# Kernel optimization log

Hardware: AMD Instinct MI355X
Metric: run time of the kernel (lower is better)

Reference implementation:

```python
import jax, jax.numpy as jnp
import numpy as np

B, T, C, H = 2, 2048, 2048, 16
HD = C // H


def setup_inputs() -> dict:
    key = jax.random.key(0)
    ks = jax.random.split(key, 5)
    s = 0.02  # init scale for weights
    return {
        "x": jax.random.normal(ks[0], (B, T, C), jnp.float32),
        "Wq": jax.random.normal(ks[1], (C, C), jnp.float32) * s,
        "Wk": jax.random.normal(ks[2], (C, C), jnp.float32) * s,
        "Wv": jax.random.normal(ks[3], (C, C), jnp.float32) * s,
        "Wo": jax.random.normal(ks[4], (C, C), jnp.float32) * s,
        "bo": jnp.zeros((C,), jnp.float32),
    }


def _alibi_slopes(n_head):
    # power-of-2 path of _get_alibi_slopes (n_head=16 is a power of 2)
    return jnp.array([1.0 / 2 ** (i + 1) for i in range(n_head)], jnp.float32)


def reference(x, Wq, Wk, Wv, Wo, bo):
    b, t, c = x.shape
    h, hd = H, HD
    scale = 1.0 / np.sqrt(hd)
    # nn.Linear (no bias): y = x @ W.T; split heads -> (B,H,T,HD)
    q = (x @ Wq.T).reshape(b, t, h, hd).transpose(0, 2, 1, 3)
    k = (x @ Wk.T).reshape(b, t, h, hd).transpose(0, 2, 1, 3)
    v = (x @ Wv.T).reshape(b, t, h, hd).transpose(0, 2, 1, 3)
    scores = jnp.einsum("bhtd,bhsd->bhts", q, k) * scale  # (B,H,T,T)
    pos = jnp.arange(t)
    diff = pos[:, None] - pos[None, :]  # (T,T), i-j
    slopes = _alibi_slopes(h)
    bias = slopes[:, None, None] * diff.astype(jnp.float32)  # (H,T,T)
    causal = diff >= 0  # lower-triangular mask
    bias = jnp.where(causal[None, :, :], bias, -jnp.inf)
    scores = scores + bias[None]  # (B,H,T,T)
    attn = jax.nn.softmax(scores, axis=-1)  # dropout = identity (eval mode)
    out = jnp.einsum("bhts,bhsd->bhtd", attn, v)
    out = out.transpose(0, 2, 1, 3).reshape(b, t, c)
    out = out @ Wo.T + bo  # proj_dropout = identity (eval mode)
    return out, attn
```

## Files before the change

kernel.cpp:

```cpp
#include <hip/hip_runtime.h>
#include <hip/hip_bf16.h>

#define DEVINL __device__ __forceinline__

typedef __attribute__((ext_vector_type(8))) short bf16x8;
typedef __attribute__((ext_vector_type(4))) float f32x4;

DEVINL ushort f2bf(float f) {
  unsigned u = __float_as_uint(f);
  u += 0x7fffu + ((u >> 16) & 1u);
  return (ushort)(u >> 16);
}

DEVINL void gl_lds16(const void* g, void* lds) {
  __builtin_amdgcn_global_load_lds(
      (const __attribute__((address_space(1))) void*)g,
      (__attribute__((address_space(3))) void*)lds, 16, 0, 0);
}

DEVINL f32x4 mfma16(bf16x8 a, bf16x8 b, f32x4 c) {
  return __builtin_amdgcn_mfma_f32_16x16x32_bf16(a, b, c, 0, 0, 0);
}

__global__ __launch_bounds__(256) void cast_bf16_kernel(const float4* __restrict__ in,
                                                        ushort4* __restrict__ out, int n4) {
  int stride = (int)(gridDim.x * blockDim.x);
  for (int i = (int)(blockIdx.x * blockDim.x + threadIdx.x); i < n4; i += stride) {
    float4 v = in[i];
    out[i] = make_ushort4(f2bf(v.x), f2bf(v.y), f2bf(v.z), f2bf(v.w));
  }
}

template <int MODE>
__global__ __launch_bounds__(256) void gemm_nt(const ushort* __restrict__ A,
                                               const ushort* __restrict__ Bm,
                                               ushort* __restrict__ Qo,
                                               ushort* __restrict__ Ko,
                                               ushort* __restrict__ Vo,
                                               float* __restrict__ Fo,
                                               const float* __restrict__ bias,
                                               int M, int N, int K) {
  __shared__ __align__(16) ushort Al[2][8192];
  __shared__ __align__(16) ushort Bl[2][8192];
  const int tid = (int)threadIdx.x;
  const int l = tid & 63, w = tid >> 6;
  const int wr = w >> 1, wc = w & 1;
  const int lr = l & 15, lg = l >> 4;

  const int nwg = (int)(gridDim.x * gridDim.y);
  const int flat = (int)(blockIdx.y * gridDim.x + blockIdx.x);
  const int swz = (flat & 7) * (nwg >> 3) + (flat >> 3);
  const int bx = swz % (int)gridDim.x, by = swz / (int)gridDim.x;
  const int rowT = by * 128, colT = bx * 128;

  f32x4 acc[4][4] = {};

  auto stage = [&](int kt, int buf) {
#pragma unroll
    for (int q = 0; q < 4; ++q) {
      int s = q * 256 + tid;
      int rb = s >> 7, ks = (s >> 6) & 1, sl = s & 63;
      size_t koff = (size_t)(kt + ks * 32 + (sl >> 4) * 8);
      gl_lds16(A + (size_t)(rowT + rb * 16 + (sl & 15)) * K + koff,
               &Al[buf][(size_t)(q * 256 + (tid & 192)) * 8]);
      gl_lds16(Bm + (size_t)(colT + rb * 16 + (sl & 15)) * K + koff,
               &Bl[buf][(size_t)(q * 256 + (tid & 192)) * 8]);
    }
  };

  stage(0, 0);
  __syncthreads();
  int cur = 0;
  for (int kt = 0; kt < K; kt += 64) {
    if (kt + 64 < K) stage(kt + 64, cur ^ 1);
#pragma unroll
    for (int ks = 0; ks < 2; ++ks) {
      bf16x8 af[4], bfv[4];
#pragma unroll
      for (int i = 0; i < 4; ++i) {
        af[i]  = *(const bf16x8*)(&Al[cur][(((wr * 4 + i) * 2 + ks) * 64 + l) * 8]);
        bfv[i] = *(const bf16x8*)(&Bl[cur][(((wc * 4 + i) * 2 + ks) * 64 + l) * 8]);
      }
#pragma unroll
      for (int i = 0; i < 4; ++i)
#pragma unroll
        for (int j = 0; j < 4; ++j)
          acc[i][j] = mfma16(af[i], bfv[j], acc[i][j]);
    }
    __syncthreads();
    cur ^= 1;
  }

  const int seg = colT >> 11;
#pragma unroll
  for (int i = 0; i < 4; ++i) {
#pragma unroll
    for (int j = 0; j < 4; ++j) {
      const int col = colT + wc * 64 + j * 16 + lr;
#pragma unroll
      for (int e = 0; e < 4; ++e) {
        const int row = rowT + wr * 64 + i * 16 + lg * 4 + e;
        float v = acc[i][j][e];
        if (MODE == 3) {
          const int c = col & 2047;
          if (seg == 0)      Qo[(size_t)row * 2048 + c] = f2bf(v);
          else if (seg == 1) Ko[(size_t)row * 2048 + c] = f2bf(v);
          else               Vo[((size_t)((row >> 11) * 2048 + c)) * 2048 + (row & 2047)] = f2bf(v);
        } else {
          Fo[(size_t)row * 2048 + col] = v + bias[col];
        }
      }
    }
  }
}

__global__ __launch_bounds__(256) void flash_kernel(const ushort* __restrict__ Qg,
                                                    const ushort* __restrict__ Kg,
                                                    const ushort* __restrict__ Vt,
                                                    ushort* __restrict__ Og,
                                                    float2* __restrict__ stats) {
  __shared__ __align__(16) ushort Kl[2][8192];
  __shared__ __align__(16) ushort Vl[2][8192];
  __shared__ __align__(16) ushort Pl[4][1024];

  const int flat = (int)(blockIdx.y * gridDim.x + blockIdx.x);
  const int swz = (flat & 7) * 64 + (flat >> 3);
  const int bx = swz & 15, bh = swz >> 4;
  const int b = bh >> 4, h = bh & 15;
  const int tid = (int)threadIdx.x, l = tid & 63, w = tid >> 6;
  const int lr = l & 15, lg = l >> 4;
  const float scale = 0.08838834764831845f;
  const float slope = exp2f(-(float)(h + 1));
  const ushort* Kbase = Kg + ((size_t)b * 2048) * 2048 + h * 128;
  const ushort* Vbase = Vt + ((size_t)b * 2048 + h * 128) * 2048;

  for (int half = 0; half < 2; ++half) {
    const int qb = (half == 0) ? 31 - bx : bx;
    const int qr0 = qb * 64 + w * 16;

    bf16x8 qf[4];
#pragma unroll
    for (int ks = 0; ks < 4; ++ks)
      qf[ks] = *(const bf16x8*)(Qg + ((size_t)b * 2048 + qr0 + lr) * 2048 + h * 128 + ks * 32 + lg * 8);

    float runmax[4], runsum[4];
    f32x4 o[8] = {};
#pragma unroll
    for (int j = 0; j < 4; ++j) { runmax[j] = -__builtin_inff(); runsum[j] = 0.f; }

    auto stage = [&](int jt, int buf) {
#pragma unroll
      for (int q = 0; q < 4; ++q) {
        const int s = q * 256 + tid;
        const int sl = s & 63;
        const int cb = s >> 8, ks = (s >> 6) & 3;
        gl_lds16(Kbase + (size_t)(jt * 64 + cb * 16 + (sl & 15)) * 2048 + ks * 32 + (sl >> 4) * 8,
                 &Kl[buf][(size_t)(q * 256 + (tid & 192)) * 8]);
        const int db = s >> 7, k2 = (s >> 6) & 1;
        gl_lds16(Vbase + (size_t)(db * 16 + (sl & 15)) * 2048 + jt * 64 + k2 * 32 + (sl >> 4) * 8,
                 &Vl[buf][(size_t)(q * 256 + (tid & 192)) * 8]);
      }
    };

    stage(qb, 0);
    __syncthreads();

    for (int jt = qb; jt >= 0; --jt) {
      const int cur = (qb - jt) & 1;
      if (jt > 0) stage(jt - 1, cur ^ 1);

      f32x4 sc[4];
      __builtin_amdgcn_s_setprio(1);
#pragma unroll
      for (int cb = 0; cb < 4; ++cb) {
        f32x4 a = {};
#pragma unroll
        for (int ks = 0; ks < 4; ++ks) {
          bf16x8 kf = *(const bf16x8*)(&Kl[cur][((cb * 4 + ks) * 64 + l) * 8]);
          a = mfma16(qf[ks], kf, a);
        }
        sc[cb] = a;
      }
      __builtin_amdgcn_s_setprio(0);
#pragma unroll
      for (int cb = 0; cb < 4; ++cb) {
        const int kj = jt * 64 + cb * 16 + lr;
#pragma unroll
        for (int j = 0; j < 4; ++j) {
          const int qi = qr0 + lg * 4 + j;
          sc[cb][j] = (kj <= qi) ? sc[cb][j] * scale + slope * (float)(qi - kj) : -__builtin_inff();
        }
      }

      float nm[4];
      bool need = false;
#pragma unroll
      for (int j = 0; j < 4; ++j) {
        float m = fmaxf(fmaxf(sc[0][j], sc[1][j]), fmaxf(sc[2][j], sc[3][j]));
#pragma unroll
        for (int d = 1; d < 16; d <<= 1) m = fmaxf(m, __shfl_xor(m, d));
        nm[j] = fmaxf(runmax[j], m);
        need = need || (nm[j] > runmax[j]);
      }
      if (__any(need)) {
#pragma unroll
        for (int j = 0; j < 4; ++j) {
          const float f = __expf(runmax[j] - nm[j]);
          runsum[j] *= f;
#pragma unroll
          for (int db = 0; db < 8; ++db) o[db][j] *= f;
          runmax[j] = nm[j];
        }
      }

#pragma unroll
      for (int cb = 0; cb < 4; ++cb) {
        const int kc = cb * 16 + lr;
#pragma unroll
        for (int j = 0; j < 4; ++j) {
          const float p = __expf(sc[cb][j] - runmax[j]);
          runsum[j] += p;
          const int l2 = (((kc & 31) >> 3) << 4) | (lg * 4 + j);
          Pl[w][((kc >> 5) * 64 + l2) * 8 + (kc & 7)] = f2bf(p);
        }
      }

      bf16x8 pf0 = *(const bf16x8*)(&Pl[w][(size_t)l * 8]);
      bf16x8 pf1 = *(const bf16x8*)(&Pl[w][(size_t)(64 + l) * 8]);
      __builtin_amdgcn_s_setprio(1);
#pragma unroll
      for (int db = 0; db < 8; ++db) {
        o[db] = mfma16(pf0, *(const bf16x8*)(&Vl[cur][((db * 2 + 0) * 64 + l) * 8]), o[db]);
        o[db] = mfma16(pf1, *(const bf16x8*)(&Vl[cur][((db * 2 + 1) * 64 + l) * 8]), o[db]);
      }
      __builtin_amdgcn_s_setprio(0);
      __syncthreads();
    }

#pragma unroll
    for (int j = 0; j < 4; ++j) {
      float s = runsum[j];
#pragma unroll
      for (int d = 1; d < 16; d <<= 1) s += __shfl_xor(s, d);
      const float iv = 1.0f / s;
      if (lr == 0) stats[(size_t)bh * 2048 + qr0 + lg * 4 + j] = make_float2(runmax[j], iv);
#pragma unroll
      for (int db = 0; db < 8; ++db) o[db][j] *= iv;
    }
#pragma unroll
    for (int db = 0; db < 8; ++db)
#pragma unroll
      for (int j = 0; j < 4; ++j)
        Og[((size_t)b * 2048 + qr0 + lg * 4 + j) * 2048 + h * 128 + db * 16 + lr] = f2bf(o[db][j]);
  }
}

__global__ __launch_bounds__(256) void probs_kernel(const ushort* __restrict__ Qg,
                                                    const ushort* __restrict__ Kg,
                                                    const float2* __restrict__ stats,
                                                    float* __restrict__ attn_out) {
  const int kb = (int)blockIdx.x, qb = (int)blockIdx.y, bh = (int)blockIdx.z;
  const int tid = (int)threadIdx.x;

  if (kb > qb) {
    float* base = attn_out + ((size_t)bh * 2048 + qb * 128) * 2048 + kb * 128;
    const float4 z = make_float4(0.f, 0.f, 0.f, 0.f);
#pragma unroll
    for (int it = 0; it < 16; ++it) {
      const int idx = it * 256 + tid;
      *(float4*)(base + (size_t)(idx >> 5) * 2048 + (idx & 31) * 4) = z;
    }
    return;
  }

  __shared__ __align__(16) ushort Ql[16384];
  __shared__ __align__(16) ushort Kl[16384];
  const int b = bh >> 4, h = bh & 15;
  const int l = tid & 63, w = tid >> 6;
  const int wr = w >> 1, wc = w & 1;
  const int lr = l & 15, lg = l >> 4;
  const float scale = 0.08838834764831845f;
  const float slope = exp2f(-(float)(h + 1));

#pragma unroll
  for (int q = 0; q < 8; ++q) {
    const int s = q * 256 + tid;
    const int sl = s & 63, rb = s >> 8, ks = (s >> 6) & 3;
    const size_t koff = (size_t)(h * 128 + ks * 32 + (sl >> 4) * 8);
    gl_lds16(Qg + ((size_t)b * 2048 + qb * 128 + rb * 16 + (sl & 15)) * 2048 + koff,
             Ql + (size_t)(q * 256 + (tid & 192)) * 8);
    gl_lds16(Kg + ((size_t)b * 2048 + kb * 128 + rb * 16 + (sl & 15)) * 2048 + koff,
             Kl + (size_t)(q * 256 + (tid & 192)) * 8);
  }
  __syncthreads();

  f32x4 acc[4][4] = {};
#pragma unroll
  for (int ks = 0; ks < 4; ++ks) {
    bf16x8 af[4], bfv[4];
#pragma unroll
    for (int i = 0; i < 4; ++i) {
      af[i]  = *(const bf16x8*)(Ql + (((wr * 4 + i) * 4 + ks) * 64 + l) * 8);
      bfv[i] = *(const bf16x8*)(Kl + (((wc * 4 + i) * 4 + ks) * 64 + l) * 8);
    }
#pragma unroll
    for (int i = 0; i < 4; ++i)
#pragma unroll
      for (int j = 0; j < 4; ++j)
        acc[i][j] = mfma16(af[i], bfv[j], acc[i][j]);
  }

  float2 st[4][4];
#pragma unroll
  for (int i = 0; i < 4; ++i)
#pragma unroll
    for (int e = 0; e < 4; ++e)
      st[i][e] = stats[(size_t)bh * 2048 + qb * 128 + wr * 64 + i * 16 + lg * 4 + e];

#pragma unroll
  for (int i = 0; i < 4; ++i) {
#pragma unroll
    for (int j = 0; j < 4; ++j) {
      const int kj = kb * 128 + wc * 64 + j * 16 + lr;
#pragma unroll
      for (int e = 0; e < 4; ++e) {
        const int qi = qb * 128 + wr * 64 + i * 16 + lg * 4 + e;
        const float sv = acc[i][j][e] * scale + slope * (float)(qi - kj);
        float p = __expf(sv - st[i][e].x) * st[i][e].y;
        if (kj > qi) p = 0.f;
        attn_out[((size_t)bh * 2048 + qi) * 2048 + kj] = p;
      }
    }
  }
}

extern "C" void kernel_launch(void* const* d_in, const int* in_sizes, int n_in,
                              void* d_out, int out_size, void* d_ws, size_t ws_size,
                              hipStream_t stream) {
  (void)in_sizes; (void)n_in; (void)out_size; (void)ws_size;
  const float* x  = (const float*)d_in[0];
  const float* Wq = (const float*)d_in[1];
  const float* Wk = (const float*)d_in[2];
  const float* Wv = (const float*)d_in[3];
  const float* Wo = (const float*)d_in[4];
  const float* bo = (const float*)d_in[5];

  float* outp  = (float*)d_out;
  float* attnp = outp + (size_t)4096 * 2048;

  char* ws = (char*)d_ws;
  ushort* xb   = (ushort*)(ws);
  ushort* wqkv = (ushort*)(ws + (16ull << 20));
  ushort* wob  = (ushort*)(ws + (40ull << 20));
  ushort* Qb   = (ushort*)(ws + (48ull << 20));
  ushort* Kb   = (ushort*)(ws + (64ull << 20));
  ushort* Vtb  = (ushort*)(ws + (80ull << 20));
  ushort* Ob   = (ushort*)(ws + (96ull << 20));
  float2* stats = (float2*)(ws);

  cast_bf16_kernel<<<2048, 256, 0, stream>>>((const float4*)x,  (ushort4*)xb, 8388608 / 4);
  cast_bf16_kernel<<<1024, 256, 0, stream>>>((const float4*)Wq, (ushort4*)(wqkv),               4194304 / 4);
  cast_bf16_kernel<<<1024, 256, 0, stream>>>((const float4*)Wk, (ushort4*)(wqkv + 4194304),     4194304 / 4);
  cast_bf16_kernel<<<1024, 256, 0, stream>>>((const float4*)Wv, (ushort4*)(wqkv + 2 * 4194304), 4194304 / 4);
  cast_bf16_kernel<<<1024, 256, 0, stream>>>((const float4*)Wo, (ushort4*)wob, 4194304 / 4);

  gemm_nt<3><<<dim3(48, 32), 256, 0, stream>>>(xb, wqkv, Qb, Kb, Vtb, nullptr, nullptr,
                                               4096, 6144, 2048);

  flash_kernel<<<dim3(16, 32), 256, 0, stream>>>(Qb, Kb, Vtb, Ob, stats);
  probs_kernel<<<dim3(16, 16, 32), 256, 0, stream>>>(Qb, Kb, stats, attnp);

  gemm_nt<2><<<dim3(16, 32), 256, 0, stream>>>(Ob, wob, nullptr, nullptr, nullptr, outp, bo,
                                               4096, 2048, 2048);
}
```

Measured before the change: 575.2 us.

## Merge cast launches, widen flash blocks to 128 query rows, nontemporal prob stores

Replaces five separate fp32-to-bf16 cast launches with a single kernel that picks its source by block index. The flash kernel goes to 512 threads covering 128 query rows per block, so each staged K/V tile is shared by eight waves, and waves skip tiles lying entirely above the causal diagonal. The max reduction across lanes now runs only when some lane's max grows. Attention-probability stores, including the zero fill, become nontemporal to avoid polluting the cache. The trade-off is that waves near the diagonal sit idle at barriers, and occupancy may drop with the larger blocks.

Measured after the change: 615.5 us. 7.0% more time.

```diff
diff --git a/kernel.cpp b/kernel.cpp
--- a/kernel.cpp
+++ b/kernel.cpp
@@ -22,12 +22,31 @@
   return __builtin_amdgcn_mfma_f32_16x16x32_bf16(a, b, c, 0, 0, 0);
 }
 
-__global__ __launch_bounds__(256) void cast_bf16_kernel(const float4* __restrict__ in,
-                                                        ushort4* __restrict__ out, int n4) {
-  int stride = (int)(gridDim.x * blockDim.x);
-  for (int i = (int)(blockIdx.x * blockDim.x + threadIdx.x); i < n4; i += stride) {
-    float4 v = in[i];
-    out[i] = make_ushort4(f2bf(v.x), f2bf(v.y), f2bf(v.z), f2bf(v.w));
+__global__ __launch_bounds__(256) void cast_all_kernel(const float4* __restrict__ x,
+                                                       const float4* __restrict__ wq,
+                                                       const float4* __restrict__ wk,
+                                                       const float4* __restrict__ wv,
+                                                       const float4* __restrict__ wo,
+                                                       ushort4* __restrict__ xb,
+                                                       ushort4* __restrict__ wqb,
+                                                       ushort4* __restrict__ wkb,
+                                                       ushort4* __restrict__ wvb,
+                                                       ushort4* __restrict__ wob) {
+  const int blk = (int)blockIdx.x;
+  const float4* src;
+  ushort4* dst;
+  int base;
+  if (blk < 2048)      { src = x;  dst = xb;  base = blk; }
+  else if (blk < 3072) { src = wq; dst = wqb; base = blk - 2048; }
+  else if (blk < 4096) { src = wk; dst = wkb; base = blk - 3072; }
+  else if (blk < 5120) { src = wv; dst = wvb; base = blk - 4096; }
+  else                 { src = wo; dst = wob; base = blk - 5120; }
+  const int idx0 = base * 1024 + (int)threadIdx.x;
+#pragma unroll
+  for (int i = 0; i < 4; ++i) {
+    const int idx = idx0 + i * 256;
+    float4 v = src[idx];
+    dst[idx] = make_ushort4(f2bf(v.x), f2bf(v.y), f2bf(v.z), f2bf(v.w));
   }
 }
 
@@ -114,14 +133,14 @@
   }
 }
 
-__global__ __launch_bounds__(256) void flash_kernel(const ushort* __restrict__ Qg,
+__global__ __launch_bounds__(512) void flash_kernel(const ushort* __restrict__ Qg,
                                                     const ushort* __restrict__ Kg,
                                                     const ushort* __restrict__ Vt,
                                                     ushort* __restrict__ Og,
                                                     float2* __restrict__ stats) {
   __shared__ __align__(16) ushort Kl[2][8192];
   __shared__ __align__(16) ushort Vl[2][8192];
-  __shared__ __align__(16) ushort Pl[4][1024];
+  __shared__ __align__(16) ushort Pl[8][1024];
 
   const int flat = (int)(blockIdx.y * gridDim.x + blockIdx.x);
   const int swz = (flat & 7) * 64 + (flat >> 3);
@@ -134,9 +153,24 @@
   const ushort* Kbase = Kg + ((size_t)b * 2048) * 2048 + h * 128;
   const ushort* Vbase = Vt + ((size_t)b * 2048 + h * 128) * 2048;
 
+  auto stage = [&](int jt, int buf) {
+#pragma unroll
+    for (int q = 0; q < 2; ++q) {
+      const int s = q * 512 + tid;
+      const int sl = s & 63;
+      const int cb = s >> 8, ks = (s >> 6) & 3;
+      gl_lds16(Kbase + (size_t)(jt * 64 + cb * 16 + (sl & 15)) * 2048 + ks * 32 + (sl >> 4) * 8,
+               &Kl[buf][(size_t)(q * 512 + (tid & 448)) * 8]);
+      const int db = s >> 7, k2 = (s >> 6) & 1;
+      gl_lds16(Vbase + (size_t)(db * 16 + (sl & 15)) * 2048 + jt * 64 + k2 * 32 + (sl >> 4) * 8,
+               &Vl[buf][(size_t)(q * 512 + (tid & 448)) * 8]);
+    }
+  };
+
   for (int half = 0; half < 2; ++half) {
-    const int qb = (half == 0) ? 31 - bx : bx;
-    const int qr0 = qb * 64 + w * 16;
+    const int q128 = (half == 0) ? 15 - bx : bx;
+    const int qr0 = q128 * 128 + w * 16;
+    const int jtmax = 2 * q128 + 1;
 
     bf16x8 qf[4];
 #pragma unroll
@@ -146,94 +180,83 @@
     float runmax[4], runsum[4];
     f32x4 o[8] = {};
 #pragma unroll
-    for (int j = 0; j < 4; ++j) { runmax[j] = -__builtin_inff(); runsum[j] = 0.f; }
-
-    auto stage = [&](int jt, int buf) {
-#pragma unroll
-      for (int q = 0; q < 4; ++q) {
-        const int s = q * 256 + tid;
-        const int sl = s & 63;
-        const int cb = s >> 8, ks = (s >> 6) & 3;
-        gl_lds16(Kbase + (size_t)(jt * 64 + cb * 16 + (sl & 15)) * 2048 + ks * 32 + (sl >> 4) * 8,
-                 &Kl[buf][(size_t)(q * 256 + (tid & 192)) * 8]);
-        const int db = s >> 7, k2 = (s >> 6) & 1;
-        gl_lds16(Vbase + (size_t)(db * 16 + (sl & 15)) * 2048 + jt * 64 + k2 * 32 + (sl >> 4) * 8,
-                 &Vl[buf][(size_t)(q * 256 + (tid & 192)) * 8]);
+    for (int j = 0; j < 4; ++j) { runmax[j] = -1e30f; runsum[j] = 0.f; }
+
+    stage(jtmax, 0);
+    __syncthreads();
+
+    for (int jt = jtmax; jt >= 0; --jt) {
+      const int cur = (jtmax - jt) & 1;
+      if (jt > 0) stage(jt - 1, cur ^ 1);
+
+      if (qr0 + 15 >= jt * 64) {
+        f32x4 sc[4];
+        __builtin_amdgcn_s_setprio(1);
+#pragma unroll
+        for (int cb = 0; cb < 4; ++cb) {
+          f32x4 a = {};
+#pragma unroll
+          for (int ks = 0; ks < 4; ++ks) {
+            bf16x8 kf = *(const bf16x8*)(&Kl[cur][((cb * 4 + ks) * 64 + l) * 8]);
+            a = mfma16(qf[ks], kf, a);
+          }
+          sc[cb] = a;
+        }
+        __builtin_amdgcn_s_setprio(0);
+#pragma unroll
+        for (int cb = 0; cb < 4; ++cb) {
+          const int kj = jt * 64 + cb * 16 + lr;
+#pragma unroll
+          for (int j = 0; j < 4; ++j) {
+            const int qi = qr0 + lg * 4 + j;
+            sc[cb][j] = (kj <= qi) ? sc[cb][j] * scale + slope * (float)(qi - kj) : -__builtin_inff();
+          }
+        }
+
+        float ml[4];
+        bool grow = false;
+#pragma unroll
+        for (int j = 0; j < 4; ++j) {
+          ml[j] = fmaxf(fmaxf(sc[0][j], sc[1][j]), fmaxf(sc[2][j], sc[3][j]));
+          grow = grow || (ml[j] > runmax[j]);
+        }
+        if (__any(grow)) {
+#pragma unroll
+          for (int j = 0; j < 4; ++j) {
+            float m = ml[j];
+#pragma unroll
+            for (int d = 1; d < 16; d <<= 1) m = fmaxf(m, __shfl_xor(m, d));
+            const float nm = fmaxf(runmax[j], m);
+            const float f = __expf(runmax[j] - nm);
+            runsum[j] *= f;
+#pragma unroll
+            for (int db = 0; db < 8; ++db) o[db][j] *= f;
+            runmax[j] = nm;
+          }
+        }
+
+#pragma unroll
+        for (int cb = 0; cb < 4; ++cb) {
+          const int kc = cb * 16 + lr;
+#pragma unroll
+          for (int j = 0; j < 4; ++j) {
+            const float p = __expf(sc[cb][j] - runmax[j]);
+            runsum[j] += p;
+            const int l2 = (((kc & 31) >> 3) << 4) | (lg * 4 + j);
+            Pl[w][((kc >> 5) * 64 + l2) * 8 + (kc & 7)] = f2bf(p);
+          }
+        }
+
+        bf16x8 pf0 = *(const bf16x8*)(&Pl[w][(size_t)l * 8]);
+        bf16x8 pf1 = *(const bf16x8*)(&Pl[w][(size_t)(64 + l) * 8]);
+        __builtin_amdgcn_s_setprio(1);
+#pragma unroll
+        for (int db = 0; db < 8; ++db) {
+          o[db] = mfma16(pf0, *(const bf16x8*)(&Vl[cur][((db * 2 + 0) * 64 + l) * 8]), o[db]);
+          o[db] = mfma16(pf1, *(const bf16x8*)(&Vl[cur][((db * 2 + 1) * 64 + l) * 8]), o[db]);
+        }
+        __builtin_amdgcn_s_setprio(0);
       }
-    };
-
-    stage(qb, 0);
-    __syncthreads();
-
-    for (int jt = qb; jt >= 0; --jt) {
-      const int cur = (qb - jt) & 1;
-      if (jt > 0) stage(jt - 1, cur ^ 1);
-
-      f32x4 sc[4];
-      __builtin_amdgcn_s_setprio(1);
-#pragma unroll
-      for (int cb = 0; cb < 4; ++cb) {
-        f32x4 a = {};
-#pragma unroll
-        for (int ks = 0; ks < 4; ++ks) {
-          bf16x8 kf = *(const bf16x8*)(&Kl[cur][((cb * 4 + ks) * 64 + l) * 8]);
-          a = mfma16(qf[ks], kf, a);
-        }
-        sc[cb] = a;
-      }
-      __builtin_amdgcn_s_setprio(0);
-#pragma unroll
-      for (int cb = 0; cb < 4; ++cb) {
-        const int kj = jt * 64 + cb * 16 + lr;
-#pragma unroll
-        for (int j = 0; j < 4; ++j) {
-          const int qi = qr0 + lg * 4 + j;
-          sc[cb][j] = (kj <= qi) ? sc[cb][j] * scale + slope * (float)(qi - kj) : -__builtin_inff();
-        }
-      }
-
-      float nm[4];
-      bool need = false;
-#pragma unroll
-      for (int j = 0; j < 4; ++j) {
-        float m = fmaxf(fmaxf(sc[0][j], sc[1][j]), fmaxf(sc[2][j], sc[3][j]));
-#pragma unroll
-        for (int d = 1; d < 16; d <<= 1) m = fmaxf(m, __shfl_xor(m, d));
-        nm[j] = fmaxf(runmax[j], m);
-        need = need || (nm[j] > runmax[j]);
-      }
-      if (__any(need)) {
-#pragma unroll
-        for (int j = 0; j < 4; ++j) {
-          const float f = __expf(runmax[j] - nm[j]);
-          runsum[j] *= f;
-#pragma unroll
-          for (int db = 0; db < 8; ++db) o[db][j] *= f;
-          runmax[j] = nm[j];
-        }
-      }
-
-#pragma unroll
-      for (int cb = 0; cb < 4; ++cb) {
-        const int kc = cb * 16 + lr;
-#pragma unroll
-        for (int j = 0; j < 4; ++j) {
-          const float p = __expf(sc[cb][j] - runmax[j]);
-          runsum[j] += p;
-          const int l2 = (((kc & 31) >> 3) << 4) | (lg * 4 + j);
-          Pl[w][((kc >> 5) * 64 + l2) * 8 + (kc & 7)] = f2bf(p);
-        }
-      }
-
-      bf16x8 pf0 = *(const bf16x8*)(&Pl[w][(size_t)l * 8]);
-      bf16x8 pf1 = *(const bf16x8*)(&Pl[w][(size_t)(64 + l) * 8]);
-      __builtin_amdgcn_s_setprio(1);
-#pragma unroll
-      for (int db = 0; db < 8; ++db) {
-        o[db] = mfma16(pf0, *(const bf16x8*)(&Vl[cur][((db * 2 + 0) * 64 + l) * 8]), o[db]);
-        o[db] = mfma16(pf1, *(const bf16x8*)(&Vl[cur][((db * 2 + 1) * 64 + l) * 8]), o[db]);
-      }
-      __builtin_amdgcn_s_setprio(0);
       __syncthreads();
     }
 
@@ -264,11 +287,11 @@
 
   if (kb > qb) {
     float* base = attn_out + ((size_t)bh * 2048 + qb * 128) * 2048 + kb * 128;
-    const float4 z = make_float4(0.f, 0.f, 0.f, 0.f);
+    const f32x4 z = {0.f, 0.f, 0.f, 0.f};
 #pragma unroll
     for (int it = 0; it < 16; ++it) {
       const int idx = it * 256 + tid;
-      *(float4*)(base + (size_t)(idx >> 5) * 2048 + (idx & 31) * 4) = z;
+      __builtin_nontemporal_store(z, (f32x4*)(base + (size_t)(idx >> 5) * 2048 + (idx & 31) * 4));
     }
     return;
   }
@@ -328,7 +351,7 @@
         const float sv = acc[i][j][e] * scale + slope * (float)(qi - kj);
         float p = __expf(sv - st[i][e].x) * st[i][e].y;
         if (kj > qi) p = 0.f;
-        attn_out[((size_t)bh * 2048 + qi) * 2048 + kj] = p;
+        __builtin_nontemporal_store(p, &attn_out[((size_t)bh * 2048 + qi) * 2048 + kj]);
       }
     }
   }
@@ -358,16 +381,15 @@
   ushort* Ob   = (ushort*)(ws + (96ull << 20));
   float2* stats = (float2*)(ws);
 
-  cast_bf16_kernel<<<2048, 256, 0, stream>>>((const float4*)x,  (ushort4*)xb, 8388608 / 4);
-  cast_bf16_kernel<<<1024, 256, 0, stream>>>((const float4*)Wq, (ushort4*)(wqkv),               4194304 / 4);
-  cast_bf16_kernel<<<1024, 256, 0, stream>>>((const float4*)Wk, (ushort4*)(wqkv + 4194304),     4194304 / 4);
-  cast_bf16_kernel<<<1024, 256, 0, stream>>>((const float4*)Wv, (ushort4*)(wqkv + 2 * 4194304), 4194304 / 4);
-  cast_bf16_kernel<<<1024, 256, 0, stream>>>((const float4*)Wo, (ushort4*)wob, 4194304 / 4);
+  cast_all_kernel<<<6144, 256, 0, stream>>>(
+      (const float4*)x, (const float4*)Wq, (const float4*)Wk, (const float4*)Wv,
+      (const float4*)Wo, (ushort4*)xb, (ushort4*)wqkv, (ushort4*)(wqkv + 4194304),
+      (ushort4*)(wqkv + 2 * 4194304), (ushort4*)wob);
 
   gemm_nt<3><<<dim3(48, 32), 256, 0, stream>>>(xb, wqkv, Qb, Kb, Vtb, nullptr, nullptr,
                                                4096, 6144, 2048);
 
-  flash_kernel<<<dim3(16, 32), 256, 0, stream>>>(Qb, Kb, Vtb, Ob, stats);
+  flash_kernel<<<dim3(16, 32), 512, 0, stream>>>(Qb, Kb, Vtb, Ob, stats);
   probs_kernel<<<dim3(16, 16, 32), 256, 0, stream>>>(Qb, Kb, stats, attnp);
 
   gemm_nt<2><<<dim3(16, 32), 256, 0, stream>>>(Ob, wob, nullptr, nullptr, nullptr, outp, bo,
```
